# Kernel tuning notes

Measured on AMD Instinct MI355X. Metric: run time of the kernel, lower is better.

## Reference

```python
import jax, jax.numpy as jnp
import numpy as np

N_NODES = 100000
N_GRAPHS = 256
EPS = 1e-5


def setup_inputs() -> dict:
    key = jax.random.key(0)
    ks = jax.random.split(key, 16)
    x = jax.random.normal(ks[0], (N_NODES, 7), dtype=jnp.float32)
    edge_index = jax.random.randint(ks[1], (2, 1600000), 0, N_NODES, dtype=jnp.int64)
    batch = jnp.sort(jax.random.randint(ks[2], (N_NODES,), 0, N_GRAPHS, dtype=jnp.int64))

    def lin(k, fi, fo):
        s = 1.0 / np.sqrt(fi)
        kw, kb = jax.random.split(k)
        W = jax.random.uniform(kw, (fi, fo), jnp.float32, -s, s)
        b = jax.random.uniform(kb, (fo,), jnp.float32, -s, s)
        return W, b

    W1, b1 = lin(ks[3], 7, 71)
    W2, b2 = lin(ks[4], 71, 135)
    W3, b3 = lin(ks[5], 135, 199)
    Wl1, bl1 = lin(ks[6], 199, 49)
    Wl2, bl2 = lin(ks[7], 49, 2)
    return {
        "x": x, "edge_index": edge_index, "batch": batch,
        "bn0_g": jnp.ones((7,)), "bn0_b": jnp.zeros((7,)),
        "bn1_g": jnp.ones((71,)), "bn1_b": jnp.zeros((71,)),
        "bn2_g": jnp.ones((135,)), "bn2_b": jnp.zeros((135,)),
        "W1": W1, "b1": b1, "W2": W2, "b2": b2, "W3": W3, "b3": b3,
        "Wl1": Wl1, "bl1": bl1, "Wl2": Wl2, "bl2": bl2,
    }


def _bn(x, g, b):
    # BatchNorm1d in training mode: batch stats over node dim
    m = jnp.mean(x, axis=0)
    v = jnp.mean(jnp.square(x - m), axis=0)
    return (x - m) * jax.lax.rsqrt(v + EPS) * g + b


def _gcn(x, src, dst, norm, W, b):
    # PyG GCNConv: x' = D^{-1/2} (A+I) D^{-1/2} (x W) + b
    h = x @ W
    out = jax.ops.segment_sum(norm[:, None] * h[src], dst, num_segments=N_NODES)
    return out + b


def reference(x, edge_index, batch, bn0_g, bn0_b, bn1_g, bn1_b, bn2_g, bn2_b,
              W1, b1, W2, b2, W3, b3, Wl1, bl1, Wl2, bl2):
    # add self loops
    loops = jnp.arange(N_NODES, dtype=edge_index.dtype)
    src = jnp.concatenate([edge_index[0], loops])
    dst = jnp.concatenate([edge_index[1], loops])
    deg = jax.ops.segment_sum(jnp.ones_like(dst, dtype=x.dtype), dst, num_segments=N_NODES)
    d_isqrt = jax.lax.rsqrt(jnp.maximum(deg, 1.0))
    norm = d_isqrt[src] * d_isqrt[dst]

    h = _bn(x, bn0_g, bn0_b)
    h = jax.nn.relu(_gcn(h, src, dst, norm, W1, b1))
    h = _bn(h, bn1_g, bn1_b)
    h = jax.nn.relu(_gcn(h, src, dst, norm, W2, b2))
    h = _bn(h, bn2_g, bn2_b)
    h = jax.nn.relu(_gcn(h, src, dst, norm, W3, b3))

    # global mean pool over graphs
    sums = jax.ops.segment_sum(h, batch, num_segments=N_GRAPHS)
    cnts = jax.ops.segment_sum(jnp.ones((h.shape[0],), h.dtype), batch, num_segments=N_GRAPHS)
    pooled = sums / jnp.maximum(cnts, 1.0)[:, None]

    out = pooled @ Wl1 + bl1
    out = out @ Wl2 + bl2
    return out
```

## Files before the change

kernel.cpp:

```cpp
#include <hip/hip_runtime.h>
#include <hip/hip_fp16.h>

#define EPSV 1e-5f
#define BIN_CH 4096
#define BCAP 8192

typedef _Float16 f16;
typedef f16 half8 __attribute__((ext_vector_type(8)));
typedef float f32x4 __attribute__((ext_vector_type(4)));


__global__ __launch_bounds__(256) void k_bin(const int* __restrict__ src,
                                             const int* __restrict__ dst, int E, int EN,
                                             int NBK, int* __restrict__ gcur,
                                             int* __restrict__ binned) {
    __shared__ int cnt[512];
    __shared__ int base[512];
    for (int b = threadIdx.x; b < 512; b += 256) cnt[b] = 0;
    __syncthreads();
    int i0 = blockIdx.x * BIN_CH;
    int i1 = i0 + BIN_CH; if (i1 > EN) i1 = EN;
    for (int i = i0 + threadIdx.x; i < i1; i += 256) {
        int d = (i < E) ? dst[i] : (i - E);
        atomicAdd(&cnt[d >> 8], 1);
    }
    __syncthreads();
    for (int b = threadIdx.x; b < NBK; b += 256)
        if (cnt[b]) base[b] = b * BCAP + atomicAdd(&gcur[b], cnt[b]);
    __syncthreads();
    for (int i = i0 + threadIdx.x; i < i1; i += 256) {
        int s, d;
        if (i < E) { s = src[i]; d = dst[i]; }
        else       { s = i - E; d = s; }
        int pos = atomicAdd(&base[d >> 8], 1);
        binned[pos] = s | ((d & 255) << 24);
    }
}

__global__ __launch_bounds__(256) void k_bucket(const int* __restrict__ binned,
                                                const int* __restrict__ gcur, int N,
                                                int* __restrict__ deg, int* __restrict__ rs,
                                                int* __restrict__ csr_s,
                                                float* __restrict__ disq) {
    __shared__ int deg_l[256];
    __shared__ int sc[256];
    __shared__ int cur_l[256];
    int b = blockIdx.x;
    int t = threadIdx.x;
    int start = b * BCAP, end = start + gcur[b];
    deg_l[t] = 0;
    __syncthreads();
    for (int i = start + t; i < end; i += 256)
        atomicAdd(&deg_l[((unsigned)binned[i]) >> 24], 1);
    __syncthreads();
    sc[t] = deg_l[t];
    __syncthreads();
    for (int off = 1; off < 256; off <<= 1) {
        int v = (t >= off) ? sc[t - off] : 0;
        __syncthreads();
        sc[t] += v;
        __syncthreads();
    }
    int rs_l = sc[t] - deg_l[t];
    int n = b * 256 + t;
    if (n < N) {
        deg[n] = deg_l[t];
        rs[n] = start + rs_l;
        disq[n] = rsqrtf((float)(deg_l[t] > 0 ? deg_l[t] : 1));
    }
    cur_l[t] = start + rs_l;
    __syncthreads();
    for (int i = start + t; i < end; i += 256) {
        int p = binned[i];
        int loc = ((unsigned)p) >> 24;
        int idx = atomicAdd(&cur_l[loc], 1);
        csr_s[idx] = p & 0xFFFFFF;
    }
}

__global__ __launch_bounds__(256) void k_wfill(const int* __restrict__ rs,
                                               const int* __restrict__ deg,
                                               const int* __restrict__ csr_s,
                                               const float* __restrict__ disq,
                                               float* __restrict__ csr_w, int N) {
    int wave = threadIdx.x >> 6, lane = threadIdx.x & 63;
    int n = blockIdx.x * 4 + wave;
    if (n >= N) return;
    int e0 = rs[n], dg = deg[n];
    float dn = disq[n];
    for (int j = lane; j < dg; j += 64) {
        int s = csr_s[e0 + j];
        csr_w[e0 + j] = disq[s] * dn;
    }
}


__global__ __launch_bounds__(256) void k_prep(
    const float* __restrict__ colsum, const float* __restrict__ colsq,
    const float* __restrict__ g, const float* __restrict__ b, float invN,
    const float* __restrict__ W, int Cin, int Cout, int KP,
    f16* __restrict__ Wp, float* __restrict__ wrow) {
    __shared__ float lsc[192];
    __shared__ float lsh[192];
    __shared__ float red[4];
    int t = threadIdx.x;
    int c = blockIdx.x;
    if (t < KP) {
        float scv = 0.f, shv = 0.f;
        if (t < Cin) {
            float m = colsum[t] * invN;
            float v = colsq[t] * invN - m * m;
            float rstd = rsqrtf(fmaxf(v, 0.f) + EPSV);
            scv = rstd * g[t];
            shv = b[t] - m * scv;
        }
        lsc[t] = scv; lsh[t] = shv;
    }
    __syncthreads();
    float part = 0.f;
    if (t < KP) {
        float wv = (t < Cin && c < Cout) ? W[(size_t)t * Cout + c] : 0.f;
        Wp[(size_t)c * KP + t] = (f16)(lsc[t] * wv);
        part = lsh[t] * wv;
    }
    for (int off = 32; off > 0; off >>= 1) part += __shfl_down(part, off);
    int lane = t & 63, wid = t >> 6;
    if (lane == 0) red[wid] = part;
    __syncthreads();
    if (t == 0) wrow[c] = red[0] + red[1] + red[2] + red[3];
}


__global__ __launch_bounds__(256) void k_padx_stats(const float* __restrict__ x,
                                                    __half* __restrict__ xp, int N,
                                                    float* __restrict__ colsum,
                                                    float* __restrict__ colsq,
                                                    const int* __restrict__ batch,
                                                    int* __restrict__ gstart,
                                                    int* __restrict__ gend) {
    __shared__ float ls[16];
    int t = threadIdx.x;
    int n = blockIdx.x * 256 + t;
    int lane = t & 63;
    if (t < 16) ls[t] = 0.f;
    __syncthreads();
    float v[7] = {0.f, 0.f, 0.f, 0.f, 0.f, 0.f, 0.f};
    if (n < N) {
#pragma unroll
        for (int j = 0; j < 7; ++j) v[j] = x[(size_t)n * 7 + j];
        __half h[8];
#pragma unroll
        for (int j = 0; j < 7; ++j) h[j] = __float2half(v[j]);
        h[7] = __float2half(0.f);
        *(float4*)(xp + (size_t)n * 8) = *(float4*)h;
        int g = batch[n];
        int gp = (n == 0) ? -1 : batch[n - 1];
        if (gp != g) gstart[g] = n;
        int gn = (n == N - 1) ? -1 : batch[n + 1];
        if (gn != g) gend[g] = n + 1;
    }
#pragma unroll
    for (int j = 0; j < 7; ++j) {
        float s = v[j];
        float q = v[j] * v[j];
        for (int off = 32; off > 0; off >>= 1) {
            s += __shfl_down(s, off);
            q += __shfl_down(q, off);
        }
        if (lane == 0) {
            atomicAdd(&ls[j], s);
            atomicAdd(&ls[8 + j], q);
        }
    }
    __syncthreads();
    if (t < 8)               atomicAdd(&colsum[t], ls[t]);
    else if (t < 16)         atomicAdd(&colsq[t - 8], ls[t]);
}


__global__ void k_gather8(const __half* __restrict__ xp, const int* __restrict__ csr_s,
                          const float* __restrict__ csr_w,
                          const int* __restrict__ rs, const int* __restrict__ deg,
                          __half* __restrict__ out, float* __restrict__ rsum, int N) {
    int n = blockIdx.x * blockDim.x + threadIdx.x;
    if (n >= N) return;
    int e0 = rs[n], eend = e0 + deg[n];
    float a0 = 0.f, a1 = 0.f, a2 = 0.f, a3 = 0.f, a4 = 0.f, a5 = 0.f, a6 = 0.f, a7 = 0.f;
    float ws = 0.f;
    for (int e = e0; e < eend; ++e) {
        int s = csr_s[e];
        float w = csr_w[e];
        ws += w;
        float4 r = *(const float4*)(xp + (size_t)s * 8);
        const __half2* hh = (const __half2*)&r;
        float2 q0 = __half22float2(hh[0]);
        float2 q1 = __half22float2(hh[1]);
        float2 q2 = __half22float2(hh[2]);
        float2 q3 = __half22float2(hh[3]);
        a0 = fmaf(w, q0.x, a0); a1 = fmaf(w, q0.y, a1);
        a2 = fmaf(w, q1.x, a2); a3 = fmaf(w, q1.y, a3);
        a4 = fmaf(w, q2.x, a4); a5 = fmaf(w, q2.y, a5);
        a6 = fmaf(w, q3.x, a6); a7 = fmaf(w, q3.y, a7);
    }
    rsum[n] = ws;
    __half h[8];
    h[0] = __float2half(a0); h[1] = __float2half(a1);
    h[2] = __float2half(a2); h[3] = __float2half(a3);
    h[4] = __float2half(a4); h[5] = __float2half(a5);
    h[6] = __float2half(a6); h[7] = __float2half(a7);
    *(float4*)(out + (size_t)n * 8) = *(float4*)h;
}

__global__ __launch_bounds__(256) void k_gather_tail(
    const __half* __restrict__ At, const int* __restrict__ csr_s,
    const float* __restrict__ csr_w, const int* __restrict__ rs,
    const int* __restrict__ deg, __half* __restrict__ out, int SPo, int coff, int N) {
    int n = blockIdx.x * blockDim.x + threadIdx.x;
    if (n >= N) return;
    int e0 = rs[n], eend = e0 + deg[n];
    float a0 = 0.f, a1 = 0.f, a2 = 0.f, a3 = 0.f, a4 = 0.f, a5 = 0.f, a6 = 0.f, a7 = 0.f;
    for (int e = e0; e < eend; ++e) {
        int s = csr_s[e];
        float w = csr_w[e];
        float4 r = *(const float4*)(At + (size_t)s * 8);
        const __half2* hh = (const __half2*)&r;
        float2 q0 = __half22float2(hh[0]);
        float2 q1 = __half22float2(hh[1]);
        float2 q2 = __half22float2(hh[2]);
        float2 q3 = __half22float2(hh[3]);
        a0 = fmaf(w, q0.x, a0); a1 = fmaf(w, q0.y, a1);
        a2 = fmaf(w, q1.x, a2); a3 = fmaf(w, q1.y, a3);
        a4 = fmaf(w, q2.x, a4); a5 = fmaf(w, q2.y, a5);
        a6 = fmaf(w, q3.x, a6); a7 = fmaf(w, q3.y, a7);
    }
    __half2 h[4];
    h[0] = __floats2half2_rn(a0, a1);
    h[1] = __floats2half2_rn(a2, a3);
    h[2] = __floats2half2_rn(a4, a5);
    h[3] = __floats2half2_rn(a6, a7);
    *(float4*)(out + (size_t)n * SPo + coff) = *(float4*)h;
}

__global__ __launch_bounds__(256) void k_gather_w(
    const __half* __restrict__ Am, int SPm, int SH,
    const int* __restrict__ rs, const int* __restrict__ deg,
    const int* __restrict__ csr_s, const float* __restrict__ csr_w,
    __half* __restrict__ out, int SPo, int N) {
    int wave = threadIdx.x >> 6;
    int lane = threadIdx.x & 63;
    int sub = lane >> SH;
    int lsub = lane & ((1 << SH) - 1);
    int npw = 64 >> SH;
    int n = (blockIdx.x * 4 + wave) * npw + sub;
    bool active = (n < N);
    int e0 = 0, eend = 0;
    if (active) { e0 = rs[n]; eend = e0 + deg[n]; }
    const __half* base = Am + lsub * 8;
    float acc[8] = {};

    int e = e0;
    for (; e + 8 <= eend; e += 8) {
        int s[8]; float wv[8]; float4 r[8];
#pragma unroll
        for (int i = 0; i < 8; ++i) { s[i] = csr_s[e + i]; wv[i] = csr_w[e + i]; }
#pragma unroll
        for (int i = 0; i < 8; ++i) r[i] = *(const float4*)(base + (size_t)s[i] * SPm);
#pragma unroll
        for (int i = 0; i < 8; ++i) {
            float2 q0 = __half22float2(((const __half2*)&r[i])[0]);
            float2 q1 = __half22float2(((const __half2*)&r[i])[1]);
            float2 q2 = __half22float2(((const __half2*)&r[i])[2]);
            float2 q3 = __half22float2(((const __half2*)&r[i])[3]);
            acc[0] = fmaf(wv[i], q0.x, acc[0]); acc[1] = fmaf(wv[i], q0.y, acc[1]);
            acc[2] = fmaf(wv[i], q1.x, acc[2]); acc[3] = fmaf(wv[i], q1.y, acc[3]);
            acc[4] = fmaf(wv[i], q2.x, acc[4]); acc[5] = fmaf(wv[i], q2.y, acc[5]);
            acc[6] = fmaf(wv[i], q3.x, acc[6]); acc[7] = fmaf(wv[i], q3.y, acc[7]);
        }
    }
    for (; e + 4 <= eend; e += 4) {
        int s[4]; float wv[4]; float4 r[4];
#pragma unroll
        for (int i = 0; i < 4; ++i) { s[i] = csr_s[e + i]; wv[i] = csr_w[e + i]; }
#pragma unroll
        for (int i = 0; i < 4; ++i) r[i] = *(const float4*)(base + (size_t)s[i] * SPm);
#pragma unroll
        for (int i = 0; i < 4; ++i) {
            float2 q0 = __half22float2(((const __half2*)&r[i])[0]);
            float2 q1 = __half22float2(((const __half2*)&r[i])[1]);
            float2 q2 = __half22float2(((const __half2*)&r[i])[2]);
            float2 q3 = __half22float2(((const __half2*)&r[i])[3]);
            acc[0] = fmaf(wv[i], q0.x, acc[0]); acc[1] = fmaf(wv[i], q0.y, acc[1]);
            acc[2] = fmaf(wv[i], q1.x, acc[2]); acc[3] = fmaf(wv[i], q1.y, acc[3]);
            acc[4] = fmaf(wv[i], q2.x, acc[4]); acc[5] = fmaf(wv[i], q2.y, acc[5]);
            acc[6] = fmaf(wv[i], q3.x, acc[6]); acc[7] = fmaf(wv[i], q3.y, acc[7]);
        }
    }
    for (; e < eend; ++e) {
        int s = csr_s[e];
        float w = csr_w[e];
        float4 r = *(const float4*)(base + (size_t)s * SPm);
        float2 q0 = __half22float2(((const __half2*)&r)[0]);
        float2 q1 = __half22float2(((const __half2*)&r)[1]);
        float2 q2 = __half22float2(((const __half2*)&r)[2]);
        float2 q3 = __half22float2(((const __half2*)&r)[3]);
        acc[0] = fmaf(w, q0.x, acc[0]); acc[1] = fmaf(w, q0.y, acc[1]);
        acc[2] = fmaf(w, q1.x, acc[2]); acc[3] = fmaf(w, q1.y, acc[3]);
        acc[4] = fmaf(w, q2.x, acc[4]); acc[5] = fmaf(w, q2.y, acc[5]);
        acc[6] = fmaf(w, q3.x, acc[6]); acc[7] = fmaf(w, q3.y, acc[7]);
    }

    if (active) {
        __half2 h[4];
        h[0] = __floats2half2_rn(acc[0], acc[1]);
        h[1] = __floats2half2_rn(acc[2], acc[3]);
        h[2] = __floats2half2_rn(acc[4], acc[5]);
        h[3] = __floats2half2_rn(acc[6], acc[7]);
        *(float4*)(out + (size_t)n * SPo + lsub * 8) = *(float4*)h;
    }
}


__global__ __launch_bounds__(256) void k_gemm_mfma(
    const f16* __restrict__ A, int SPa,
    const f16* __restrict__ Bt, int KP,
    const float* __restrict__ rsum, const float* __restrict__ wrow,
    const float* __restrict__ bias,
    f16* __restrict__ outM, int SPm, int MAIN, f16* __restrict__ outT, int TOTW,
    float* __restrict__ colsum, float* __restrict__ colsq, int do_stats,
    int N, int Cout) {
    __shared__ f16 As[128][40];
    __shared__ float s_sum[64];
    __shared__ float s_sq[64];
    const int r0 = blockIdx.x * 128;
    const int c0 = blockIdx.y * 64;
    const int t = threadIdx.x;
    const int wave = t >> 6, lane = t & 63;
    const int l15 = lane & 15, quad = lane >> 4;

    if (t < 64) { s_sum[t] = 0.f; s_sq[t] = 0.f; }

    f32x4 zero4 = {0.f, 0.f, 0.f, 0.f};
    f32x4 acc[2][4];
#pragma unroll
    for (int mi = 0; mi < 2; ++mi)
#pragma unroll
        for (int ni = 0; ni < 4; ++ni) acc[mi][ni] = zero4;

    const int KT = KP >> 5;
    for (int kt = 0; kt < KT; ++kt) {
        int k0 = kt * 32;
        {
            int kcol = (t & 7) * 4;
            int rbase = t >> 3;
            int gk = k0 + kcol;
            bool kok = (gk + 4 <= SPa);
#pragma unroll
            for (int i = 0; i < 4; ++i) {
                int row = rbase + i * 32;
                int gr = r0 + row;
                ushort4 v = {0, 0, 0, 0};
                if (gr < N && kok)
                    v = *(const ushort4*)(A + (size_t)gr * SPa + gk);
                *(ushort4*)&As[row][kcol] = v;
            }
        }
        __syncthreads();
        half8 a0 = *(const half8*)&As[wave * 32 + l15][quad * 8];
        half8 a1 = *(const half8*)&As[wave * 32 + 16 + l15][quad * 8];
#pragma unroll
        for (int ni = 0; ni < 4; ++ni) {
            half8 b = *(const half8*)(Bt + (size_t)(c0 + ni * 16 + l15) * KP + k0 + quad * 8);
            acc[0][ni] = __builtin_amdgcn_mfma_f32_16x16x32_f16(a0, b, acc[0][ni], 0, 0, 0);
            acc[1][ni] = __builtin_amdgcn_mfma_f32_16x16x32_f16(a1, b, acc[1][ni], 0, 0, 0);
        }
        __syncthreads();
    }

    float wr[4], bi[4];
#pragma unroll
    for (int ni = 0; ni < 4; ++ni) {
        int gc = c0 + ni * 16 + l15;
        wr[ni] = wrow[gc];
        bi[ni] = (gc < Cout) ? bias[gc] : 0.f;
    }
    float ps[4] = {}, pq[4] = {};
#pragma unroll
    for (int mi = 0; mi < 2; ++mi) {
#pragma unroll
        for (int reg = 0; reg < 4; ++reg) {
            int gr = r0 + wave * 32 + mi * 16 + quad * 4 + reg;
            if (gr >= N) continue;
            float rsv = rsum[gr];
#pragma unroll
            for (int ni = 0; ni < 4; ++ni) {
                int gc = c0 + ni * 16 + l15;
                float o = acc[mi][ni][reg] + rsv * wr[ni] + bi[ni];
                o = fmaxf(o, 0.f);
                if (gc >= Cout) o = 0.f;
                ps[ni] += o; pq[ni] += o * o;
                if (gc < MAIN) {
                    if (gc < TOTW) outM[(size_t)gr * SPm + gc] = (f16)o;
                } else if (gc < TOTW) {
                    outT[(size_t)gr * 8 + (gc - MAIN)] = (f16)o;
                }
            }
        }
    }
    if (do_stats) {
#pragma unroll
        for (int ni = 0; ni < 4; ++ni) {
            int cl = ni * 16 + l15;
            atomicAdd(&s_sum[cl], ps[ni]);
            atomicAdd(&s_sq[cl], pq[ni]);
        }
        __syncthreads();
        if (t < 64 && c0 + t < Cout) {
            atomicAdd(&colsum[c0 + t], s_sum[t]);
            atomicAdd(&colsq[c0 + t], s_sq[t]);
        }
    }
}


__global__ __launch_bounds__(256) void k_gemm_pool(
    const f16* __restrict__ A, int SPa,
    const f16* __restrict__ Bt, int KP,
    const float* __restrict__ rsum, const float* __restrict__ wrow,
    const float* __restrict__ bias, const int* __restrict__ batch,
    float* __restrict__ pooled, int N, int Cout) {
    __shared__ f16 As[128][40];
    __shared__ int sbat[128];
    __shared__ float s_red[4][64];
    const int r0 = blockIdx.x * 128;
    const int c0 = blockIdx.y * 64;
    const int t = threadIdx.x;
    const int wave = t >> 6, lane = t & 63;
    const int l15 = lane & 15, quad = lane >> 4;

    if (t < 128) {
        int gr = r0 + t;
        sbat[t] = batch[(gr < N) ? gr : (N - 1)];
    }

    f32x4 zero4 = {0.f, 0.f, 0.f, 0.f};
    f32x4 acc[2][4];
#pragma unroll
    for (int mi = 0; mi < 2; ++mi)
#pragma unroll
        for (int ni = 0; ni < 4; ++ni) acc[mi][ni] = zero4;

    const int KT = KP >> 5;
    for (int kt = 0; kt < KT; ++kt) {
        int k0 = kt * 32;
        {
            int kcol = (t & 7) * 4;
            int rbase = t >> 3;
            int gk = k0 + kcol;
            bool kok = (gk + 4 <= SPa);
#pragma unroll
            for (int i = 0; i < 4; ++i) {
                int row = rbase + i * 32;
                int gr = r0 + row;
                ushort4 v = {0, 0, 0, 0};
                if (gr < N && kok)
                    v = *(const ushort4*)(A + (size_t)gr * SPa + gk);
                *(ushort4*)&As[row][kcol] = v;
            }
        }
        __syncthreads();
        half8 a0 = *(const half8*)&As[wave * 32 + l15][quad * 8];
        half8 a1 = *(const half8*)&As[wave * 32 + 16 + l15][quad * 8];
#pragma unroll
        for (int ni = 0; ni < 4; ++ni) {
            half8 b = *(const half8*)(Bt + (size_t)(c0 + ni * 16 + l15) * KP + k0 + quad * 8);
            acc[0][ni] = __builtin_amdgcn_mfma_f32_16x16x32_f16(a0, b, acc[0][ni], 0, 0, 0);
            acc[1][ni] = __builtin_amdgcn_mfma_f32_16x16x32_f16(a1, b, acc[1][ni], 0, 0, 0);
        }
        __syncthreads();
    }

    float wr[4], bi[4];
#pragma unroll
    for (int ni = 0; ni < 4; ++ni) {
        int gc = c0 + ni * 16 + l15;
        wr[ni] = wrow[gc];
        bi[ni] = (gc < Cout) ? bias[gc] : 0.f;
    }
    int gid[8];
#pragma unroll
    for (int mi = 0; mi < 2; ++mi) {
#pragma unroll
        for (int reg = 0; reg < 4; ++reg) {
            int lrow = wave * 32 + mi * 16 + quad * 4 + reg;
            int gr = r0 + lrow;
            bool rok = (gr < N);
            float rsv = rok ? rsum[gr] : 0.f;
            gid[mi * 4 + reg] = sbat[lrow];
#pragma unroll
            for (int ni = 0; ni < 4; ++ni) {
                float o = acc[mi][ni][reg] + rsv * wr[ni] + bi[ni];
                o = fmaxf(o, 0.f);
                acc[mi][ni][reg] = rok ? o : 0.f;
            }
        }
    }

    const int g0 = sbat[0];
    const int gmax = sbat[127];
    for (int g = g0; g <= gmax; ++g) {
        float part[4] = {0.f, 0.f, 0.f, 0.f};
#pragma unroll
        for (int mi = 0; mi < 2; ++mi)
#pragma unroll
            for (int reg = 0; reg < 4; ++reg) {
                bool m = (gid[mi * 4 + reg] == g);
#pragma unroll
                for (int ni = 0; ni < 4; ++ni)
                    part[ni] += m ? acc[mi][ni][reg] : 0.f;
            }
#pragma unroll
        for (int ni = 0; ni < 4; ++ni) {
            part[ni] += __shfl_down(part[ni], 32);
            part[ni] += __shfl_down(part[ni], 16);
        }
        if (lane < 16) {
#pragma unroll
            for (int ni = 0; ni < 4; ++ni) s_red[wave][ni * 16 + lane] = part[ni];
        }
        __syncthreads();
        if (t < 64) {
            int gc = c0 + t;
            if (gc < Cout) {
                float v = s_red[0][t] + s_red[1][t] + s_red[2][t] + s_red[3][t];
                if (v != 0.f) atomicAdd(&pooled[(size_t)g * Cout + gc], v);
            }
        }
        __syncthreads();
    }
}


__global__ void k_mlp(const float* __restrict__ pooled, const int* __restrict__ gstart,
                      const int* __restrict__ gend,
                      const float* __restrict__ Wl1, const float* __restrict__ bl1,
                      const float* __restrict__ Wl2, const float* __restrict__ bl2,
                      float* __restrict__ out, int C) {
    __shared__ float p[199];
    __shared__ float t1[49];
    int g = blockIdx.x;
    int cnt = gend[g] - gstart[g];
    float inv = 1.f / (float)(cnt > 1 ? cnt : 1);
    for (int k = threadIdx.x; k < C; k += blockDim.x) p[k] = pooled[g * C + k] * inv;
    __syncthreads();
    if (threadIdx.x < 49) {
        float acc = bl1[threadIdx.x];
        for (int k = 0; k < C; ++k) acc += p[k] * Wl1[k * 49 + threadIdx.x];
        t1[threadIdx.x] = acc;
    }
    __syncthreads();
    if (threadIdx.x < 2) {
        float acc = bl2[threadIdx.x];
        for (int k = 0; k < 49; ++k) acc += t1[k] * Wl2[k * 2 + threadIdx.x];
        out[g * 2 + threadIdx.x] = acc;
    }
}


extern "C" void kernel_launch(void* const* d_in, const int* in_sizes, int n_in,
                              void* d_out, int out_size, void* d_ws, size_t ws_size,
                              hipStream_t stream) {
    const float* x     = (const float*)d_in[0];
    const int*   ei    = (const int*)d_in[1];
    const int*   batch = (const int*)d_in[2];
    const float* bn0g = (const float*)d_in[3];
    const float* bn0b = (const float*)d_in[4];
    const float* bn1g = (const float*)d_in[5];
    const float* bn1b = (const float*)d_in[6];
    const float* bn2g = (const float*)d_in[7];
    const float* bn2b = (const float*)d_in[8];
    const float* W1  = (const float*)d_in[9];
    const float* b1  = (const float*)d_in[10];
    const float* W2  = (const float*)d_in[11];
    const float* b2  = (const float*)d_in[12];
    const float* W3  = (const float*)d_in[13];
    const float* b3  = (const float*)d_in[14];
    const float* Wl1 = (const float*)d_in[15];
    const float* bl1 = (const float*)d_in[16];
    const float* Wl2 = (const float*)d_in[17];
    const float* bl2 = (const float*)d_in[18];

    const int N = in_sizes[0] / 7;
    const int E = in_sizes[1] / 2;
    const int EN = E + N;
    const int G = out_size / 2;
    const int NB = (N + 255) / 256;
    const int NBK = (N + 255) / 256;
    const int NBIN = (EN + BIN_CH - 1) / BIN_CH;

    const int* src = ei;
    const int* dst = ei + E;

    char* w = (char*)d_ws;
    auto alloc = [&](size_t bytes) -> void* {
        void* p = (void*)w;
        w += ((bytes + 255) / 256) * 256;
        return p;
    };
    size_t szH1m = (size_t)N * 64 * sizeof(__half);
    size_t szH1t = (size_t)N * 8 * sizeof(__half);
    size_t szH2m = (size_t)N * 128 * sizeof(__half);
    size_t szH2t = (size_t)N * 8 * sizeof(__half);
    char* regA = (char*)alloc(szH1m + szH1t + szH2m + szH2t);
    __half* H1m = (__half*)regA;
    __half* H1t = (__half*)(regA + szH1m);
    __half* H2m = (__half*)(regA + szH1m + szH1t);
    __half* H2t = (__half*)(regA + szH1m + szH1t + szH2m);

    __half* bufG = (__half*)alloc((size_t)N * 136 * sizeof(__half));
    f16*    wp   = (f16*)  alloc((size_t)256 * 160 * sizeof(f16));
    float*  wrow = (float*)alloc(256 * sizeof(float));
    __half* xp   = (__half*)alloc((size_t)N * 8 * sizeof(__half));
    float* disq  = (float*)alloc((size_t)N * sizeof(float));
    float* rsum  = (float*)alloc((size_t)N * sizeof(float));
    int*   deg   = (int*)  alloc((size_t)N * sizeof(int));
    int*   rs    = (int*)  alloc((size_t)N * sizeof(int));
    int*   binned= (int*)  alloc((size_t)NBK * BCAP * sizeof(int));
    int*   csr_s = (int*)  alloc((size_t)NBK * BCAP * sizeof(int));
    float* csr_w = (float*)alloc((size_t)NBK * BCAP * sizeof(float));
    float* colsum0 = (float*)alloc(256 * sizeof(float));
    float* colsq0  = (float*)alloc(256 * sizeof(float));
    float* colsumA = (float*)alloc(256 * sizeof(float));
    float* colsqA  = (float*)alloc(256 * sizeof(float));
    float* colsumB = (float*)alloc(256 * sizeof(float));
    float* colsqB  = (float*)alloc(256 * sizeof(float));
    int*   gcur    = (int*)  alloc(512 * sizeof(int));
    float* pooled  = (float*)alloc((size_t)G * 199 * sizeof(float));
    int*   gstart  = (int*)  alloc((size_t)G * sizeof(int));
    int*   gend    = (int*)  alloc((size_t)G * sizeof(int));

    size_t zbytes = 6 * 1024 + 2048 + (((size_t)G * 199 * sizeof(float) + 255) / 256) * 256;
    hipMemsetAsync(colsum0, 0, zbytes, stream);

    k_bin<<<NBIN, 256, 0, stream>>>(src, dst, E, EN, NBK, gcur, binned);
    k_bucket<<<NBK, 256, 0, stream>>>(binned, gcur, N, deg, rs, csr_s, disq);
    k_wfill<<<(N + 3) / 4, 256, 0, stream>>>(rs, deg, csr_s, disq, csr_w, N);

    const int GB = (N + 127) / 128;

    k_padx_stats<<<NB, 256, 0, stream>>>(x, xp, N, colsum0, colsq0, batch, gstart, gend);
    k_prep<<<128, 256, 0, stream>>>(colsum0, colsq0, bn0g, bn0b, 1.f / (float)N,
                                    W1, 7, 71, 32, wp, wrow);
    k_gather8<<<(N + 255) / 256, 256, 0, stream>>>(xp, csr_s, csr_w, rs, deg, bufG, rsum, N);
    {
        dim3 grid(GB, 2);
        k_gemm_mfma<<<grid, 256, 0, stream>>>((const f16*)bufG, 8, wp, 32, rsum, wrow, b1,
                                              (f16*)H1m, 64, 64, (f16*)H1t, 72,
                                              colsumA, colsqA, 1, N, 71);
    }
    k_prep<<<192, 256, 0, stream>>>(colsumA, colsqA, bn1g, bn1b, 1.f / (float)N,
                                    W2, 71, 135, 96, wp, wrow);
    k_gather_w<<<(N + 31) / 32, 256, 0, stream>>>(H1m, 64, 3,
                                                  rs, deg, csr_s, csr_w, bufG, 72, N);
    k_gather_tail<<<(N + 255) / 256, 256, 0, stream>>>(H1t, csr_s, csr_w, rs, deg,
                                                       bufG, 72, 64, N);
    {
        dim3 grid(GB, 3);
        k_gemm_mfma<<<grid, 256, 0, stream>>>((const f16*)bufG, 72, wp, 96, rsum, wrow, b2,
                                              (f16*)H2m, 128, 128, (f16*)H2t, 136,
                                              colsumB, colsqB, 1, N, 135);
    }
    k_prep<<<256, 256, 0, stream>>>(colsumB, colsqB, bn2g, bn2b, 1.f / (float)N,
                                    W3, 135, 199, 160, wp, wrow);
    k_gather_w<<<(N + 15) / 16, 256, 0, stream>>>(H2m, 128, 4,
                                                  rs, deg, csr_s, csr_w, bufG, 136, N);
    k_gather_tail<<<(N + 255) / 256, 256, 0, stream>>>(H2t, csr_s, csr_w, rs, deg,
                                                       bufG, 136, 128, N);
    {
        dim3 grid(GB, 4);
        k_gemm_pool<<<grid, 256, 0, stream>>>((const f16*)bufG, 136, wp, 160, rsum, wrow, b3,
                                              batch, pooled, N, 199);
    }

    k_mlp<<<G, 64, 0, stream>>>(pooled, gstart, gend, Wl1, bl1, Wl2, bl2, (float*)d_out, 199);
}
```

Before: 504.5 us.

## Fuse neighbor gather into MFMA GEMM for GCN layers two and three

Replaces the separate gather (main and tail) kernels plus the GEMM for layers 2 and 3 with single kernels. Each block gathers aggregated neighbor features for its 128 rows directly into shared memory, then runs all output column tiles with MFMA from LDS, computing BN statistics or pooled sums. This avoids writing and re-reading the intermediate gathered buffer and cuts launches. In exchange, each block holds a large LDS tile, which can lower occupancy, and the gather and GEMM phases are serialized within a block with no overlap.

```diff
diff --git a/kernel.cpp b/kernel.cpp
--- a/kernel.cpp
+++ b/kernel.cpp
@@ -211,114 +211,6 @@
     *(float4*)(out + (size_t)n * 8) = *(float4*)h;
 }
 
-__global__ __launch_bounds__(256) void k_gather_tail(
-    const __half* __restrict__ At, const int* __restrict__ csr_s,
-    const float* __restrict__ csr_w, const int* __restrict__ rs,
-    const int* __restrict__ deg, __half* __restrict__ out, int SPo, int coff, int N) {
-    int n = blockIdx.x * blockDim.x + threadIdx.x;
-    if (n >= N) return;
-    int e0 = rs[n], eend = e0 + deg[n];
-    float a0 = 0.f, a1 = 0.f, a2 = 0.f, a3 = 0.f, a4 = 0.f, a5 = 0.f, a6 = 0.f, a7 = 0.f;
-    for (int e = e0; e < eend; ++e) {
-        int s = csr_s[e];
-        float w = csr_w[e];
-        float4 r = *(const float4*)(At + (size_t)s * 8);
-        const __half2* hh = (const __half2*)&r;
-        float2 q0 = __half22float2(hh[0]);
-        float2 q1 = __half22float2(hh[1]);
-        float2 q2 = __half22float2(hh[2]);
-        float2 q3 = __half22float2(hh[3]);
-        a0 = fmaf(w, q0.x, a0); a1 = fmaf(w, q0.y, a1);
-        a2 = fmaf(w, q1.x, a2); a3 = fmaf(w, q1.y, a3);
-        a4 = fmaf(w, q2.x, a4); a5 = fmaf(w, q2.y, a5);
-        a6 = fmaf(w, q3.x, a6); a7 = fmaf(w, q3.y, a7);
-    }
-    __half2 h[4];
-    h[0] = __floats2half2_rn(a0, a1);
-    h[1] = __floats2half2_rn(a2, a3);
-    h[2] = __floats2half2_rn(a4, a5);
-    h[3] = __floats2half2_rn(a6, a7);
-    *(float4*)(out + (size_t)n * SPo + coff) = *(float4*)h;
-}
-
-__global__ __launch_bounds__(256) void k_gather_w(
-    const __half* __restrict__ Am, int SPm, int SH,
-    const int* __restrict__ rs, const int* __restrict__ deg,
-    const int* __restrict__ csr_s, const float* __restrict__ csr_w,
-    __half* __restrict__ out, int SPo, int N) {
-    int wave = threadIdx.x >> 6;
-    int lane = threadIdx.x & 63;
-    int sub = lane >> SH;
-    int lsub = lane & ((1 << SH) - 1);
-    int npw = 64 >> SH;
-    int n = (blockIdx.x * 4 + wave) * npw + sub;
-    bool active = (n < N);
-    int e0 = 0, eend = 0;
-    if (active) { e0 = rs[n]; eend = e0 + deg[n]; }
-    const __half* base = Am + lsub * 8;
-    float acc[8] = {};
-
-    int e = e0;
-    for (; e + 8 <= eend; e += 8) {
-        int s[8]; float wv[8]; float4 r[8];
-#pragma unroll
-        for (int i = 0; i < 8; ++i) { s[i] = csr_s[e + i]; wv[i] = csr_w[e + i]; }
-#pragma unroll
-        for (int i = 0; i < 8; ++i) r[i] = *(const float4*)(base + (size_t)s[i] * SPm);
-#pragma unroll
-        for (int i = 0; i < 8; ++i) {
-            float2 q0 = __half22float2(((const __half2*)&r[i])[0]);
-            float2 q1 = __half22float2(((const __half2*)&r[i])[1]);
-            float2 q2 = __half22float2(((const __half2*)&r[i])[2]);
-            float2 q3 = __half22float2(((const __half2*)&r[i])[3]);
-            acc[0] = fmaf(wv[i], q0.x, acc[0]); acc[1] = fmaf(wv[i], q0.y, acc[1]);
-            acc[2] = fmaf(wv[i], q1.x, acc[2]); acc[3] = fmaf(wv[i], q1.y, acc[3]);
-            acc[4] = fmaf(wv[i], q2.x, acc[4]); acc[5] = fmaf(wv[i], q2.y, acc[5]);
-            acc[6] = fmaf(wv[i], q3.x, acc[6]); acc[7] = fmaf(wv[i], q3.y, acc[7]);
-        }
-    }
-    for (; e + 4 <= eend; e += 4) {
-        int s[4]; float wv[4]; float4 r[4];
-#pragma unroll
-        for (int i = 0; i < 4; ++i) { s[i] = csr_s[e + i]; wv[i] = csr_w[e + i]; }
-#pragma unroll
-        for (int i = 0; i < 4; ++i) r[i] = *(const float4*)(base + (size_t)s[i] * SPm);
-#pragma unroll
-        for (int i = 0; i < 4; ++i) {
-            float2 q0 = __half22float2(((const __half2*)&r[i])[0]);
-            float2 q1 = __half22float2(((const __half2*)&r[i])[1]);
-            float2 q2 = __half22float2(((const __half2*)&r[i])[2]);
-            float2 q3 = __half22float2(((const __half2*)&r[i])[3]);
-            acc[0] = fmaf(wv[i], q0.x, acc[0]); acc[1] = fmaf(wv[i], q0.y, acc[1]);
-            acc[2] = fmaf(wv[i], q1.x, acc[2]); acc[3] = fmaf(wv[i], q1.y, acc[3]);
-            acc[4] = fmaf(wv[i], q2.x, acc[4]); acc[5] = fmaf(wv[i], q2.y, acc[5]);
-            acc[6] = fmaf(wv[i], q3.x, acc[6]); acc[7] = fmaf(wv[i], q3.y, acc[7]);
-        }
-    }
-    for (; e < eend; ++e) {
-        int s = csr_s[e];
-        float w = csr_w[e];
-        float4 r = *(const float4*)(base + (size_t)s * SPm);
-        float2 q0 = __half22float2(((const __half2*)&r)[0]);
-        float2 q1 = __half22float2(((const __half2*)&r)[1]);
-        float2 q2 = __half22float2(((const __half2*)&r)[2]);
-        float2 q3 = __half22float2(((const __half2*)&r)[3]);
-        acc[0] = fmaf(w, q0.x, acc[0]); acc[1] = fmaf(w, q0.y, acc[1]);
-        acc[2] = fmaf(w, q1.x, acc[2]); acc[3] = fmaf(w, q1.y, acc[3]);
-        acc[4] = fmaf(w, q2.x, acc[4]); acc[5] = fmaf(w, q2.y, acc[5]);
-        acc[6] = fmaf(w, q3.x, acc[6]); acc[7] = fmaf(w, q3.y, acc[7]);
-    }
-
-    if (active) {
-        __half2 h[4];
-        h[0] = __floats2half2_rn(acc[0], acc[1]);
-        h[1] = __floats2half2_rn(acc[2], acc[3]);
-        h[2] = __floats2half2_rn(acc[4], acc[5]);
-        h[3] = __floats2half2_rn(acc[6], acc[7]);
-        *(float4*)(out + (size_t)n * SPo + lsub * 8) = *(float4*)h;
-    }
-}
-
 
 __global__ __launch_bounds__(256) void k_gemm_mfma(
     const f16* __restrict__ A, int SPa,
@@ -421,18 +313,200 @@
     }
 }
 
-
-__global__ __launch_bounds__(256) void k_gemm_pool(
-    const f16* __restrict__ A, int SPa,
-    const f16* __restrict__ Bt, int KP,
+__device__ __forceinline__ void fma8(float* acc, float w, float4 r) {
+    float2 q0 = __half22float2(((const __half2*)&r)[0]);
+    float2 q1 = __half22float2(((const __half2*)&r)[1]);
+    float2 q2 = __half22float2(((const __half2*)&r)[2]);
+    float2 q3 = __half22float2(((const __half2*)&r)[3]);
+    acc[0] = fmaf(w, q0.x, acc[0]); acc[1] = fmaf(w, q0.y, acc[1]);
+    acc[2] = fmaf(w, q1.x, acc[2]); acc[3] = fmaf(w, q1.y, acc[3]);
+    acc[4] = fmaf(w, q2.x, acc[4]); acc[5] = fmaf(w, q2.y, acc[5]);
+    acc[6] = fmaf(w, q3.x, acc[6]); acc[7] = fmaf(w, q3.y, acc[7]);
+}
+
+
+__global__ __launch_bounds__(256) void k_fused2(
+    const __half* __restrict__ Am, const __half* __restrict__ At,
+    const f16* __restrict__ Bt,
+    const int* __restrict__ rs, const int* __restrict__ deg,
+    const int* __restrict__ csr_s, const float* __restrict__ csr_w,
+    const float* __restrict__ rsum, const float* __restrict__ wrow,
+    const float* __restrict__ bias,
+    f16* __restrict__ outM, f16* __restrict__ outT,
+    float* __restrict__ colsum, float* __restrict__ colsq, int N) {
+    const int KP = 96, ASW = 104, SPM = 64, COUT = 135;
+    __shared__ f16 As[128][104];
+    __shared__ float s_red[4][64];
+    __shared__ float s_red2[4][64];
+    const int r0 = blockIdx.x * 128;
+    const int t = threadIdx.x;
+    const int wave = t >> 6, lane = t & 63;
+    const int l15 = lane & 15, quad = lane >> 4;
+
+    {
+        float4 z = {0.f, 0.f, 0.f, 0.f};
+        for (int i = t; i < 128 * ASW / 8; i += 256) ((float4*)As)[i] = z;
+    }
+    __syncthreads();
+
+    {
+        const int sub = lane >> 3, lsub = lane & 7;
+        const __half* gb = Am + lsub * 8;
+        for (int pass = 0; pass < 4; ++pass) {
+            int lrow = wave * 32 + pass * 8 + sub;
+            int n = r0 + lrow;
+            float acc[8] = {};
+            if (n < N) {
+                int e0 = rs[n], eend = e0 + deg[n];
+                int e = e0;
+                for (; e + 8 <= eend; e += 8) {
+                    int s[8]; float wv[8]; float4 r[8];
+#pragma unroll
+                    for (int i = 0; i < 8; ++i) { s[i] = csr_s[e + i]; wv[i] = csr_w[e + i]; }
+#pragma unroll
+                    for (int i = 0; i < 8; ++i) r[i] = *(const float4*)(gb + (size_t)s[i] * SPM);
+#pragma unroll
+                    for (int i = 0; i < 8; ++i) fma8(acc, wv[i], r[i]);
+                }
+                for (; e + 4 <= eend; e += 4) {
+                    int s[4]; float wv[4]; float4 r[4];
+#pragma unroll
+                    for (int i = 0; i < 4; ++i) { s[i] = csr_s[e + i]; wv[i] = csr_w[e + i]; }
+#pragma unroll
+                    for (int i = 0; i < 4; ++i) r[i] = *(const float4*)(gb + (size_t)s[i] * SPM);
+#pragma unroll
+                    for (int i = 0; i < 4; ++i) fma8(acc, wv[i], r[i]);
+                }
+                for (; e < eend; ++e)
+                    fma8(acc, csr_w[e], *(const float4*)(gb + (size_t)csr_s[e] * SPM));
+            }
+            __half2 h[4];
+            h[0] = __floats2half2_rn(acc[0], acc[1]);
+            h[1] = __floats2half2_rn(acc[2], acc[3]);
+            h[2] = __floats2half2_rn(acc[4], acc[5]);
+            h[3] = __floats2half2_rn(acc[6], acc[7]);
+            *(float4*)&As[lrow][lsub * 8] = *(float4*)h;
+        }
+    }
+    {
+        const int p = lane >> 1, half = lane & 1;
+        int lrow = wave * 32 + p;
+        int n = r0 + lrow;
+        float acc[8] = {};
+        if (n < N) {
+            int eend = rs[n] + deg[n];
+            int e = rs[n] + half;
+            for (; e + 6 < eend; e += 8) {
+                int s0 = csr_s[e], s1 = csr_s[e + 2], s2 = csr_s[e + 4], s3 = csr_s[e + 6];
+                float w0 = csr_w[e], w1 = csr_w[e + 2], w2 = csr_w[e + 4], w3 = csr_w[e + 6];
+                float4 r0_ = *(const float4*)(At + (size_t)s0 * 8);
+                float4 r1_ = *(const float4*)(At + (size_t)s1 * 8);
+                float4 r2_ = *(const float4*)(At + (size_t)s2 * 8);
+                float4 r3_ = *(const float4*)(At + (size_t)s3 * 8);
+                fma8(acc, w0, r0_); fma8(acc, w1, r1_);
+                fma8(acc, w2, r2_); fma8(acc, w3, r3_);
+            }
+            for (; e < eend; e += 2)
+                fma8(acc, csr_w[e], *(const float4*)(At + (size_t)csr_s[e] * 8));
+        }
+#pragma unroll
+        for (int j = 0; j < 8; ++j) acc[j] += __shfl_xor(acc[j], 1);
+        if (half == 0) {
+            __half2 h[4];
+            h[0] = __floats2half2_rn(acc[0], acc[1]);
+            h[1] = __floats2half2_rn(acc[2], acc[3]);
+            h[2] = __floats2half2_rn(acc[4], acc[5]);
+            h[3] = __floats2half2_rn(acc[6], acc[7]);
+            *(float4*)&As[lrow][64] = *(float4*)h;
+        }
+    }
+    __syncthreads();
+
+    for (int ct = 0; ct < 3; ++ct) {
+        const int c0 = ct * 64;
+        f32x4 zero4 = {0.f, 0.f, 0.f, 0.f};
+        f32x4 acc2[2][4];
+#pragma unroll
+        for (int mi = 0; mi < 2; ++mi)
+#pragma unroll
+            for (int ni = 0; ni < 4; ++ni) acc2[mi][ni] = zero4;
+#pragma unroll
+        for (int kt = 0; kt < 3; ++kt) {
+            int k0 = kt * 32;
+            half8 a0 = *(const half8*)&As[wave * 32 + l15][k0 + quad * 8];
+            half8 a1 = *(const half8*)&As[wave * 32 + 16 + l15][k0 + quad * 8];
+#pragma unroll
+            for (int ni = 0; ni < 4; ++ni) {
+                half8 b = *(const half8*)(Bt + (size_t)(c0 + ni * 16 + l15) * KP + k0 + quad * 8);
+                acc2[0][ni] = __builtin_amdgcn_mfma_f32_16x16x32_f16(a0, b, acc2[0][ni], 0, 0, 0);
+                acc2[1][ni] = __builtin_amdgcn_mfma_f32_16x16x32_f16(a1, b, acc2[1][ni], 0, 0, 0);
+            }
+        }
+        float wr[4], bi[4];
+#pragma unroll
+        for (int ni = 0; ni < 4; ++ni) {
+            int gc = c0 + ni * 16 + l15;
+            wr[ni] = wrow[gc];
+            bi[ni] = (gc < COUT) ? bias[gc] : 0.f;
+        }
+        float ps[4] = {}, pq[4] = {};
+#pragma unroll
+        for (int mi = 0; mi < 2; ++mi) {
+#pragma unroll
+            for (int reg = 0; reg < 4; ++reg) {
+                int gr = r0 + wave * 32 + mi * 16 + quad * 4 + reg;
+                if (gr >= N) continue;
+                float rsv = rsum[gr];
+#pragma unroll
+                for (int ni = 0; ni < 4; ++ni) {
+                    int gc = c0 + ni * 16 + l15;
+                    float o = acc2[mi][ni][reg] + rsv * wr[ni] + bi[ni];
+                    o = fmaxf(o, 0.f);
+                    if (gc >= COUT) o = 0.f;
+                    ps[ni] += o; pq[ni] += o * o;
+                    if (gc < 128)      outM[(size_t)gr * 128 + gc] = (f16)o;
+                    else if (gc < 136) outT[(size_t)gr * 8 + (gc - 128)] = (f16)o;
+                }
+            }
+        }
+#pragma unroll
+        for (int ni = 0; ni < 4; ++ni) {
+            ps[ni] += __shfl_down(ps[ni], 32); ps[ni] += __shfl_down(ps[ni], 16);
+            pq[ni] += __shfl_down(pq[ni], 32); pq[ni] += __shfl_down(pq[ni], 16);
+        }
+        if (lane < 16) {
+#pragma unroll
+            for (int ni = 0; ni < 4; ++ni) {
+                s_red[wave][ni * 16 + lane] = ps[ni];
+                s_red2[wave][ni * 16 + lane] = pq[ni];
+            }
+        }
+        __syncthreads();
+        if (t < 64) {
+            int gc = c0 + t;
+            if (gc < COUT) {
+                atomicAdd(&colsum[gc], s_red[0][t] + s_red[1][t] + s_red[2][t] + s_red[3][t]);
+                atomicAdd(&colsq[gc], s_red2[0][t] + s_red2[1][t] + s_red2[2][t] + s_red2[3][t]);
+            }
+        }
+        __syncthreads();
+    }
+}
+
+
+__global__ __launch_bounds__(256) void k_fused3(
+    const __half* __restrict__ Am, const __half* __restrict__ At,
+    const f16* __restrict__ Bt,
+    const int* __restrict__ rs, const int* __restrict__ deg,
+    const int* __restrict__ csr_s, const float* __restrict__ csr_w,
     const float* __restrict__ rsum, const float* __restrict__ wrow,
     const float* __restrict__ bias, const int* __restrict__ batch,
-    float* __restrict__ pooled, int N, int Cout) {
-    __shared__ f16 As[128][40];
+    float* __restrict__ pooled, int N) {
+    const int KP = 160, ASW = 168, SPM = 128, COUT = 199;
+    __shared__ f16 As[128][168];
     __shared__ int sbat[128];
     __shared__ float s_red[4][64];
     const int r0 = blockIdx.x * 128;
-    const int c0 = blockIdx.y * 64;
     const int t = threadIdx.x;
     const int wave = t >> 6, lane = t & 63;
     const int l15 = lane & 15, quad = lane >> 4;
@@ -441,101 +515,170 @@
         int gr = r0 + t;
         sbat[t] = batch[(gr < N) ? gr : (N - 1)];
     }
-
-    f32x4 zero4 = {0.f, 0.f, 0.f, 0.f};
-    f32x4 acc[2][4];
+    {
+        float4 z = {0.f, 0.f, 0.f, 0.f};
+        for (int i = t; i < 128 * ASW / 8; i += 256) ((float4*)As)[i] = z;
+    }
+    __syncthreads();
+
+    {
+        const int sub = lane >> 4, lsub = lane & 15;
+        const __half* gb = Am + lsub * 8;
+        for (int pass = 0; pass < 8; ++pass) {
+            int lrow = wave * 32 + pass * 4 + sub;
+            int n = r0 + lrow;
+            float acc[8] = {};
+            if (n < N) {
+                int e0 = rs[n], eend = e0 + deg[n];
+                int e = e0;
+                for (; e + 8 <= eend; e += 8) {
+                    int s[8]; float wv[8]; float4 r[8];
+#pragma unroll
+                    for (int i = 0; i < 8; ++i) { s[i] = csr_s[e + i]; wv[i] = csr_w[e + i]; }
+#pragma unroll
+                    for (int i = 0; i < 8; ++i) r[i] = *(const float4*)(gb + (size_t)s[i] * SPM);
+#pragma unroll
+                    for (int i = 0; i < 8; ++i) fma8(acc, wv[i], r[i]);
+                }
+                for (; e + 4 <= eend; e += 4) {
+                    int s[4]; float wv[4]; float4 r[4];
+#pragma unroll
+                    for (int i = 0; i < 4; ++i) { s[i] = csr_s[e + i]; wv[i] = csr_w[e + i]; }
+#pragma unroll
+                    for (int i = 0; i < 4; ++i) r[i] = *(const float4*)(gb + (size_t)s[i] * SPM);
+#pragma unroll
+                    for (int i = 0; i < 4; ++i) fma8(acc, wv[i], r[i]);
+                }
+                for (; e < eend; ++e)
+                    fma8(acc, csr_w[e], *(const float4*)(gb + (size_t)csr_s[e] * SPM));
+            }
+            __half2 h[4];
+            h[0] = __floats2half2_rn(acc[0], acc[1]);
+            h[1] = __floats2half2_rn(acc[2], acc[3]);
+            h[2] = __floats2half2_rn(acc[4], acc[5]);
+            h[3] = __floats2half2_rn(acc[6], acc[7]);
+            *(float4*)&As[lrow][lsub * 8] = *(float4*)h;
+        }
+    }
+    {
+        const int p = lane >> 1, half = lane & 1;
+        int lrow = wave * 32 + p;
+        int n = r0 + lrow;
+        float acc[8] = {};
+        if (n < N) {
+            int eend = rs[n] + deg[n];
+            int e = rs[n] + half;
+            for (; e + 6 < eend; e += 8) {
+                int s0 = csr_s[e], s1 = csr_s[e + 2], s2 = csr_s[e + 4], s3 = csr_s[e + 6];
+                float w0 = csr_w[e], w1 = csr_w[e + 2], w2 = csr_w[e + 4], w3 = csr_w[e + 6];
+                float4 r0_ = *(const float4*)(At + (size_t)s0 * 8);
+                float4 r1_ = *(const float4*)(At + (size_t)s1 * 8);
+                float4 r2_ = *(const float4*)(At + (size_t)s2 * 8);
+                float4 r3_ = *(const float4*)(At + (size_t)s3 * 8);
+                fma8(acc, w0, r0_); fma8(acc, w1, r1_);
+                fma8(acc, w2, r2_); fma8(acc, w3, r3_);
+            }
+            for (; e < eend; e += 2)
+                fma8(acc, csr_w[e], *(const float4*)(At + (size_t)csr_s[e] * 8));
+        }
+#pragma unroll
+        for (int j = 0; j < 8; ++j) acc[j] += __shfl_xor(acc[j], 1);
+        if (half == 0) {
+            __half2 h[4];
+            h[0] = __floats2half2_rn(acc[0], acc[1]);
+            h[1] = __floats2half2_rn(acc[2], acc[3]);
+            h[2] = __floats2half2_rn(acc[4], acc[5]);
+            h[3] = __floats2half2_rn(acc[6], acc[7]);
+            *(float4*)&As[lrow][128] = *(float4*)h;
+        }
+    }
+    __syncthreads();
+
+    int gid[8]; float rsv8[8]; bool rok[8];
 #pragma unroll
     for (int mi = 0; mi < 2; ++mi)
-#pragma unroll
-        for (int ni = 0; ni < 4; ++ni) acc[mi][ni] = zero4;
-
-    const int KT = KP >> 5;
-    for (int kt = 0; kt < KT; ++kt) {
-        int k0 = kt * 32;
-        {
-            int kcol = (t & 7) * 4;
-            int rbase = t >> 3;
-            int gk = k0 + kcol;
-            bool kok = (gk + 4 <= SPa);
-#pragma unroll
-            for (int i = 0; i < 4; ++i) {
-                int row = rbase + i * 32;
-                int gr = r0 + row;
-                ushort4 v = {0, 0, 0, 0};
-                if (gr < N && kok)
-                    v = *(const ushort4*)(A + (size_t)gr * SPa + gk);
-                *(ushort4*)&As[row][kcol] = v;
-            }
-        }
-        __syncthreads();
-        half8 a0 = *(const half8*)&As[wave * 32 + l15][quad * 8];
-        half8 a1 = *(const half8*)&As[wave * 32 + 16 + l15][quad * 8];
-#pragma unroll
-        for (int ni = 0; ni < 4; ++ni) {
-            half8 b = *(const half8*)(Bt + (size_t)(c0 + ni * 16 + l15) * KP + k0 + quad * 8);
-            acc[0][ni] = __builtin_amdgcn_mfma_f32_16x16x32_f16(a0, b, acc[0][ni], 0, 0, 0);
-            acc[1][ni] = __builtin_amdgcn_mfma_f32_16x16x32_f16(a1, b, acc[1][ni], 0, 0, 0);
-        }
-        __syncthreads();
-    }
-
-    float wr[4], bi[4];
-#pragma unroll
-    for (int ni = 0; ni < 4; ++ni) {
-        int gc = c0 + ni * 16 + l15;
-        wr[ni] = wrow[gc];
-        bi[ni] = (gc < Cout) ? bias[gc] : 0.f;
-    }
-    int gid[8];
-#pragma unroll
-    for (int mi = 0; mi < 2; ++mi) {
 #pragma unroll
         for (int reg = 0; reg < 4; ++reg) {
             int lrow = wave * 32 + mi * 16 + quad * 4 + reg;
             int gr = r0 + lrow;
-            bool rok = (gr < N);
-            float rsv = rok ? rsum[gr] : 0.f;
-            gid[mi * 4 + reg] = sbat[lrow];
-#pragma unroll
-            for (int ni = 0; ni < 4; ++ni) {
-                float o = acc[mi][ni][reg] + rsv * wr[ni] + bi[ni];
-                o = fmaxf(o, 0.f);
-                acc[mi][ni][reg] = rok ? o : 0.f;
-            }
-        }
-    }
-
+            int idx = mi * 4 + reg;
+            gid[idx] = sbat[lrow];
+            rok[idx] = (gr < N);
+            rsv8[idx] = rok[idx] ? rsum[gr] : 0.f;
+        }
     const int g0 = sbat[0];
     const int gmax = sbat[127];
-    for (int g = g0; g <= gmax; ++g) {
-        float part[4] = {0.f, 0.f, 0.f, 0.f};
+
+    for (int ct = 0; ct < 4; ++ct) {
+        const int c0 = ct * 64;
+        f32x4 zero4 = {0.f, 0.f, 0.f, 0.f};
+        f32x4 acc2[2][4];
 #pragma unroll
         for (int mi = 0; mi < 2; ++mi)
 #pragma unroll
+            for (int ni = 0; ni < 4; ++ni) acc2[mi][ni] = zero4;
+#pragma unroll
+        for (int kt = 0; kt < 5; ++kt) {
+            int k0 = kt * 32;
+            half8 a0 = *(const half8*)&As[wave * 32 + l15][k0 + quad * 8];
+            half8 a1 = *(const half8*)&As[wave * 32 + 16 + l15][k0 + quad * 8];
+#pragma unroll
+            for (int ni = 0; ni < 4; ++ni) {
+                half8 b = *(const half8*)(Bt + (size_t)(c0 + ni * 16 + l15) * KP + k0 + quad * 8);
+                acc2[0][ni] = __builtin_amdgcn_mfma_f32_16x16x32_f16(a0, b, acc2[0][ni], 0, 0, 0);
+                acc2[1][ni] = __builtin_amdgcn_mfma_f32_16x16x32_f16(a1, b, acc2[1][ni], 0, 0, 0);
+            }
+        }
+        float wr[4], bi[4];
+#pragma unroll
+        for (int ni = 0; ni < 4; ++ni) {
+            int gc = c0 + ni * 16 + l15;
+            wr[ni] = wrow[gc];
+            bi[ni] = (gc < COUT) ? bias[gc] : 0.f;
+        }
+#pragma unroll
+        for (int mi = 0; mi < 2; ++mi)
+#pragma unroll
             for (int reg = 0; reg < 4; ++reg) {
-                bool m = (gid[mi * 4 + reg] == g);
-#pragma unroll
-                for (int ni = 0; ni < 4; ++ni)
-                    part[ni] += m ? acc[mi][ni][reg] : 0.f;
-            }
-#pragma unroll
-        for (int ni = 0; ni < 4; ++ni) {
-            part[ni] += __shfl_down(part[ni], 32);
-            part[ni] += __shfl_down(part[ni], 16);
-        }
-        if (lane < 16) {
-#pragma unroll
-            for (int ni = 0; ni < 4; ++ni) s_red[wave][ni * 16 + lane] = part[ni];
-        }
-        __syncthreads();
-        if (t < 64) {
-            int gc = c0 + t;
-            if (gc < Cout) {
-                float v = s_red[0][t] + s_red[1][t] + s_red[2][t] + s_red[3][t];
-                if (v != 0.f) atomicAdd(&pooled[(size_t)g * Cout + gc], v);
-            }
-        }
-        __syncthreads();
+                int idx = mi * 4 + reg;
+#pragma unroll
+                for (int ni = 0; ni < 4; ++ni) {
+                    int gc = c0 + ni * 16 + l15;
+                    float o = acc2[mi][ni][reg] + rsv8[idx] * wr[ni] + bi[ni];
+                    o = fmaxf(o, 0.f);
+                    acc2[mi][ni][reg] = (rok[idx] && gc < COUT) ? o : 0.f;
+                }
+            }
+        for (int g = g0; g <= gmax; ++g) {
+            float part[4] = {0.f, 0.f, 0.f, 0.f};
+#pragma unroll
+            for (int mi = 0; mi < 2; ++mi)
+#pragma unroll
+                for (int reg = 0; reg < 4; ++reg) {
+                    bool m = (gid[mi * 4 + reg] == g);
+#pragma unroll
+                    for (int ni = 0; ni < 4; ++ni)
+                        part[ni] += m ? acc2[mi][ni][reg] : 0.f;
+                }
+#pragma unroll
+            for (int ni = 0; ni < 4; ++ni) {
+                part[ni] += __shfl_down(part[ni], 32);
+                part[ni] += __shfl_down(part[ni], 16);
+            }
+            if (lane < 16) {
+#pragma unroll
+                for (int ni = 0; ni < 4; ++ni) s_red[wave][ni * 16 + lane] = part[ni];
+            }
+            __syncthreads();
+            if (t < 64) {
+                int gc = c0 + t;
+                if (gc < COUT) {
+                    float v = s_red[0][t] + s_red[1][t] + s_red[2][t] + s_red[3][t];
+                    if (v != 0.f) atomicAdd(&pooled[(size_t)g * COUT + gc], v);
+                }
+            }
+            __syncthreads();
+        }
     }
 }
 
@@ -616,7 +759,7 @@
     __half* H2m = (__half*)(regA + szH1m + szH1t);
     __half* H2t = (__half*)(regA + szH1m + szH1t + szH2m);
 
-    __half* bufG = (__half*)alloc((size_t)N * 136 * sizeof(__half));
+    __half* bufG = (__half*)alloc((size_t)N * 8 * sizeof(__half));
     f16*    wp   = (f16*)  alloc((size_t)256 * 160 * sizeof(f16));
     float*  wrow = (float*)alloc(256 * sizeof(float));
     __half* xp   = (__half*)alloc((size_t)N * 8 * sizeof(__half));
@@ -659,27 +802,13 @@
     }
     k_prep<<<192, 256, 0, stream>>>(colsumA, colsqA, bn1g, bn1b, 1.f / (float)N,
                                     W2, 71, 135, 96, wp, wrow);
-    k_gather_w<<<(N + 31) / 32, 256, 0, stream>>>(H1m, 64, 3,
-                                                  rs, deg, csr_s, csr_w, bufG, 72, N);
-    k_gather_tail<<<(N + 255) / 256, 256, 0, stream>>>(H1t, csr_s, csr_w, rs, deg,
-                                                       bufG, 72, 64, N);
-    {
-        dim3 grid(GB, 3);
-        k_gemm_mfma<<<grid, 256, 0, stream>>>((const f16*)bufG, 72, wp, 96, rsum, wrow, b2,
-                                              (f16*)H2m, 128, 128, (f16*)H2t, 136,
-                                              colsumB, colsqB, 1, N, 135);
-    }
+    k_fused2<<<GB, 256, 0, stream>>>(H1m, H1t, wp, rs, deg, csr_s, csr_w,
+                                     rsum, wrow, b2, (f16*)H2m, (f16*)H2t,
+                                     colsumB, colsqB, N);
     k_prep<<<256, 256, 0, stream>>>(colsumB, colsqB, bn2g, bn2b, 1.f / (float)N,
                                     W3, 135, 199, 160, wp, wrow);
-    k_gather_w<<<(N + 15) / 16, 256, 0, stream>>>(H2m, 128, 4,
-                                                  rs, deg, csr_s, csr_w, bufG, 136, N);
-    k_gather_tail<<<(N + 255) / 256, 256, 0, stream>>>(H2t, csr_s, csr_w, rs, deg,
-                                                       bufG, 136, 128, N);
-    {
-        dim3 grid(GB, 4);
-        k_gemm_pool<<<grid, 256, 0, stream>>>((const f16*)bufG, 136, wp, 160, rsum, wrow, b3,
-                                              batch, pooled, N, 199);
-    }
+    k_fused3<<<GB, 256, 0, stream>>>(H2m, H2t, wp, rs, deg, csr_s, csr_w,
+                                     rsum, wrow, b3, batch, pooled, N);
 
     k_mlp<<<G, 64, 0, stream>>>(pooled, gstart, gend, Wl1, bl1, Wl2, bl2, (float*)d_out, 199);
 }
```

New measurement: 489.9 us. 1.03x faster.
